# Performance work log

Hardware: AMD Instinct MI355X
Metric: run time of the kernel (lower is better)

## Reference

```python
import jax, jax.numpy as jnp
import numpy as np

B, N, D, DN, F, NUM_F, O, H = 8, 4096, 256, 128, 128, 1024, 8, 1024
EPS = 1e-5

def setup_inputs() -> dict:
    key = jax.random.key(0)
    ks = jax.random.split(key, 10)
    s = 0.02
    x = jax.random.normal(ks[0], (B, N, D), dtype=jnp.float32)
    ctx = jax.random.normal(ks[1], (B, DN), dtype=jnp.float32)
    idx = jax.random.randint(ks[2], (F,), 0, NUM_F, dtype=jnp.int64)
    cond_w = jax.random.normal(ks[3], (DN, 2 * D), dtype=jnp.float32) * s
    cond_b = jnp.zeros((2 * D,), dtype=jnp.float32)
    ffn_w_in = jax.random.normal(ks[4], (D, 2 * H), dtype=jnp.float32) * s
    ffn_b_in = jnp.zeros((2 * H,), dtype=jnp.float32)
    ffn_w_out = jax.random.normal(ks[5], (H, D), dtype=jnp.float32) * s
    ffn_b_out = jnp.zeros((D,), dtype=jnp.float32)
    emb = jax.random.normal(ks[6], (NUM_F, D * O), dtype=jnp.float32) * s
    return {"x": x, "ctx": ctx, "idx": idx, "cond_w": cond_w, "cond_b": cond_b,
            "ffn_w_in": ffn_w_in, "ffn_b_in": ffn_b_in,
            "ffn_w_out": ffn_w_out, "ffn_b_out": ffn_b_out, "emb": emb}

def reference(x, ctx, idx, cond_w, cond_b, ffn_w_in, ffn_b_in, ffn_w_out, ffn_b_out, emb):
    # Conditional LayerNorm: normalize over last dim, FiLM-style modulation from ctx
    mu = jnp.mean(x, axis=-1, keepdims=True)
    var = jnp.mean((x - mu) ** 2, axis=-1, keepdims=True)
    h = (x - mu) * jax.lax.rsqrt(var + EPS)                      # [B,N,D]
    ss = ctx @ cond_w + cond_b                                   # [B,2D]
    scale, shift = jnp.split(ss, 2, axis=-1)                     # [B,D] each
    h = h * (1.0 + scale[:, None, :]) + shift[:, None, :]
    # Gated FFN: in-proj -> (gelu(gate) * value) -> out-proj
    uv = h @ ffn_w_in + ffn_b_in                                 # [B,N,2H]
    u, v = jnp.split(uv, 2, axis=-1)
    y = (jax.nn.gelu(u) * v) @ ffn_w_out + ffn_b_out             # [B,N,D]
    # Embedding-generated per-feature output weights, then batched contraction
    w = emb[idx].reshape(F, D, O)                                # gather [F,D,O]
    out = jnp.einsum('bnd,fdo->bnfo', y, w)                      # [B,N,F,O]
    return out
```

## Files before the change

kernel.cpp:

```cpp
#include <hip/hip_runtime.h>
#include <cstdint>
#include <cstddef>

#define M_TOT 32768
#define D_    256
#define DN_   128
#define TWO_D 512
#define H_    1024
#define TWO_H 2048

typedef unsigned short ushort_t;
typedef __attribute__((ext_vector_type(8))) short bf16x8;
typedef __attribute__((ext_vector_type(4))) float f32x4;

__device__ __forceinline__ ushort_t f2bf(float f) {
  union { float f; uint32_t i; } v; v.f = f;
  uint32_t r = v.i + 0x7fffu + ((v.i >> 16) & 1u);
  return (ushort_t)(r >> 16);
}

__device__ __forceinline__ void async_ld16(const void* g, void* l) {
  __builtin_amdgcn_global_load_lds(
      (const __attribute__((address_space(1))) void*)g,
      (__attribute__((address_space(3))) void*)l, 16, 0, 0);
}

__global__ __launch_bounds__(256) void cond_ss_kernel(
    const float* __restrict__ ctx, const float* __restrict__ cond_w,
    const float* __restrict__ cond_b, float* __restrict__ ss) {
  int j = blockIdx.x * 256 + threadIdx.x;
  int b = j >> 9, col = j & 511;
  float acc = cond_b[col];
  for (int k = 0; k < DN_; ++k)
    acc += ctx[b * DN_ + k] * cond_w[k * TWO_D + col];
  ss[j] = acc;
}

__global__ __launch_bounds__(256) void prep_kernel(
    const float* __restrict__ w_in,
    const float* __restrict__ w_out,
    const float* __restrict__ emb,
    const int* __restrict__ idx,
    ushort_t* __restrict__ WinT,
    ushort_t* __restrict__ WoutT,
    ushort_t* __restrict__ W2T) {
  int id = blockIdx.x * 256 + threadIdx.x;
  if (id < 524288) {
    int n = id >> 8, k = id & 255;
    WinT[id] = f2bf(w_in[k * TWO_H + n]);
  } else if (id < 786432) {
    int t = id - 524288;
    int n = t >> 10, k = t & 1023;
    WoutT[t] = f2bf(w_out[k * D_ + n]);
  } else {
    int t = id - 786432;
    int c = t >> 8, d = t & 255;
    int f = c >> 3, o = c & 7;
    bool looks64 = (idx[1] == 0) & (idx[3] == 0) & (idx[5] == 0) & (idx[7] == 0);
    int fi = looks64 ? idx[2 * f] : idx[f];
    W2T[t] = f2bf(emb[(size_t)fi * 2048 + d * 8 + o]);
  }
}

__global__ __launch_bounds__(256) void ln_film_kernel(
    const float* __restrict__ x, const float* __restrict__ ss,
    ushort_t* __restrict__ h) {
  int row = blockIdx.x * 4 + (threadIdx.x >> 6);
  int lane = threadIdx.x & 63;
  int b = row >> 12;
  const float* xr = x + (size_t)row * D_;
  float4 pk = *(const float4*)(xr + lane * 4);
  float f0 = pk.x, f1 = pk.y, f2 = pk.z, f3 = pk.w;
  float s = f0 + f1 + f2 + f3;
  float q = f0 * f0 + f1 * f1 + f2 * f2 + f3 * f3;
#pragma unroll
  for (int off = 32; off > 0; off >>= 1) {
    s += __shfl_xor(s, off, 64);
    q += __shfl_xor(q, off, 64);
  }
  float mean = s * (1.0f / 256.0f);
  float var = q * (1.0f / 256.0f) - mean * mean;
  float rs = rsqrtf(var + 1e-5f);
  int d = lane * 4;
  const float* ssb = ss + b * TWO_D;
  float o0 = (f0 - mean) * rs * (1.0f + ssb[d + 0]) + ssb[256 + d + 0];
  float o1 = (f1 - mean) * rs * (1.0f + ssb[d + 1]) + ssb[256 + d + 1];
  float o2 = (f2 - mean) * rs * (1.0f + ssb[d + 2]) + ssb[256 + d + 2];
  float o3 = (f3 - mean) * rs * (1.0f + ssb[d + 3]) + ssb[256 + d + 3];
  uint2 st;
  st.x = (uint32_t)f2bf(o0) | ((uint32_t)f2bf(o1) << 16);
  st.y = (uint32_t)f2bf(o2) | ((uint32_t)f2bf(o3) << 16);
  *(uint2*)(h + (size_t)row * D_ + lane * 4) = st;
}

template <bool BIAS, bool OUT_F32>
__global__ __launch_bounds__(256, 2) void gemm_bt_kernel(
    const ushort_t* __restrict__ A, const ushort_t* __restrict__ BT,
    const float* __restrict__ bias, void* __restrict__ Cout,
    int M, int N, int K) {
  __shared__ ushort_t As[128 * 32];
  __shared__ ushort_t Bs[128 * 32];
  const int tid = threadIdx.x, lane = tid & 63, wave = tid >> 6;
  const int wm = wave >> 1, wn = wave & 1;
  const int m0 = blockIdx.x * 128, n0 = blockIdx.y * 128;
  const int srow = lane >> 2, sch = (lane & 3) * 8;
  f32x4 acc[4][4] = {};
  for (int k0 = 0; k0 < K; k0 += 32) {
    for (int i = wave; i < 8; i += 4) {
      async_ld16(A + (size_t)(m0 + i * 16 + srow) * K + k0 + sch, &As[i * 512]);
      async_ld16(BT + (size_t)(n0 + i * 16 + srow) * K + k0 + sch, &Bs[i * 512]);
    }
    __syncthreads();
    bf16x8 a[4], b[4];
#pragma unroll
    for (int i = 0; i < 4; ++i)
      a[i] = *(const bf16x8*)&As[(wm * 64 + i * 16 + (lane & 15)) * 32 + (lane >> 4) * 8];
#pragma unroll
    for (int j = 0; j < 4; ++j)
      b[j] = *(const bf16x8*)&Bs[(wn * 64 + j * 16 + (lane & 15)) * 32 + (lane >> 4) * 8];
#pragma unroll
    for (int i = 0; i < 4; ++i)
#pragma unroll
      for (int j = 0; j < 4; ++j)
        acc[i][j] = __builtin_amdgcn_mfma_f32_16x16x32_bf16(a[i], b[j], acc[i][j], 0, 0, 0);
    __syncthreads();
  }
#pragma unroll
  for (int j = 0; j < 4; ++j) {
    int col = n0 + wn * 64 + j * 16 + (lane & 15);
    float bv = BIAS ? bias[col] : 0.0f;
#pragma unroll
    for (int i = 0; i < 4; ++i) {
      int rowb = m0 + wm * 64 + i * 16 + ((lane >> 4) << 2);
#pragma unroll
      for (int r = 0; r < 4; ++r) {
        float val = acc[i][j][r] + bv;
        if (OUT_F32)
          ((float*)Cout)[(size_t)(rowb + r) * N + col] = val;
        else
          ((ushort_t*)Cout)[(size_t)(rowb + r) * N + col] = f2bf(val);
      }
    }
  }
}

__global__ __launch_bounds__(256, 2) void gemm_gated_kernel(
    const ushort_t* __restrict__ A,
    const ushort_t* __restrict__ WinT,
    const float* __restrict__ bin,
    ushort_t* __restrict__ G) {
  __shared__ ushort_t As[128 * 32];
  __shared__ ushort_t Bus[64 * 32];
  __shared__ ushort_t Bvs[64 * 32];
  const int tid = threadIdx.x, lane = tid & 63, wave = tid >> 6;
  const int wm = wave >> 1, wn = wave & 1;
  const int m0 = blockIdx.x * 128;
  const int j0 = blockIdx.y * 64;
  const int srow = lane >> 2, sch = (lane & 3) * 8;
  const int K = 256;
  f32x4 au[4][2] = {}, av[4][2] = {};
  for (int k0 = 0; k0 < K; k0 += 32) {
    for (int i = wave; i < 8; i += 4)
      async_ld16(A + (size_t)(m0 + i * 16 + srow) * K + k0 + sch, &As[i * 512]);
    {
      int i = wave;
      async_ld16(WinT + (size_t)(j0 + i * 16 + srow) * K + k0 + sch, &Bus[i * 512]);
      async_ld16(WinT + (size_t)(1024 + j0 + i * 16 + srow) * K + k0 + sch, &Bvs[i * 512]);
    }
    __syncthreads();
    bf16x8 a[4], bu[2], bv[2];
#pragma unroll
    for (int i = 0; i < 4; ++i)
      a[i] = *(const bf16x8*)&As[(wm * 64 + i * 16 + (lane & 15)) * 32 + (lane >> 4) * 8];
#pragma unroll
    for (int j = 0; j < 2; ++j) {
      bu[j] = *(const bf16x8*)&Bus[(wn * 32 + j * 16 + (lane & 15)) * 32 + (lane >> 4) * 8];
      bv[j] = *(const bf16x8*)&Bvs[(wn * 32 + j * 16 + (lane & 15)) * 32 + (lane >> 4) * 8];
    }
#pragma unroll
    for (int i = 0; i < 4; ++i)
#pragma unroll
      for (int j = 0; j < 2; ++j) {
        au[i][j] = __builtin_amdgcn_mfma_f32_16x16x32_bf16(a[i], bu[j], au[i][j], 0, 0, 0);
        av[i][j] = __builtin_amdgcn_mfma_f32_16x16x32_bf16(a[i], bv[j], av[i][j], 0, 0, 0);
      }
    __syncthreads();
  }
#pragma unroll
  for (int j = 0; j < 2; ++j) {
    int col = j0 + wn * 32 + j * 16 + (lane & 15);
    float bub = bin[col];
    float bvb = bin[1024 + col];
#pragma unroll
    for (int i = 0; i < 4; ++i) {
      int rowb = m0 + wm * 64 + i * 16 + ((lane >> 4) << 2);
#pragma unroll
      for (int r = 0; r < 4; ++r) {
        float u = au[i][j][r] + bub;
        float v = av[i][j][r] + bvb;
        float t = 0.7978845608028654f * (u + 0.044715f * u * u * u);
        float e = __expf(2.0f * t);
        float th = 1.0f - 2.0f / (e + 1.0f);
        float gl = 0.5f * u * (1.0f + th);
        G[(size_t)(rowb + r) * 1024 + col] = f2bf(gl * v);
      }
    }
  }
}

extern "C" void kernel_launch(void* const* d_in, const int* in_sizes, int n_in,
                              void* d_out, int out_size, void* d_ws, size_t ws_size,
                              hipStream_t stream) {
  const float* x      = (const float*)d_in[0];
  const float* ctx    = (const float*)d_in[1];
  const int*   idx    = (const int*)d_in[2];
  const float* cond_w = (const float*)d_in[3];
  const float* cond_b = (const float*)d_in[4];
  const float* w_in   = (const float*)d_in[5];
  const float* b_in   = (const float*)d_in[6];
  const float* w_out  = (const float*)d_in[7];
  const float* b_out  = (const float*)d_in[8];
  const float* emb    = (const float*)d_in[9];

  char* w = (char*)d_ws;
  float* ss = (float*)w;           w += (size_t)8 * TWO_D * 4;
  ushort_t* h = (ushort_t*)w;      w += (size_t)M_TOT * D_ * 2;
  ushort_t* y = (ushort_t*)w;      w += (size_t)M_TOT * D_ * 2;
  ushort_t* WinT = (ushort_t*)w;   w += (size_t)TWO_H * D_ * 2;
  ushort_t* WoutT = (ushort_t*)w;  w += (size_t)D_ * H_ * 2;
  ushort_t* W2T = (ushort_t*)w;    w += (size_t)H_ * D_ * 2;
  ushort_t* g = (ushort_t*)d_out;

  cond_ss_kernel<<<16, 256, 0, stream>>>(ctx, cond_w, cond_b, ss);
  prep_kernel<<<4096, 256, 0, stream>>>(w_in, w_out, emb, idx, WinT, WoutT, W2T);
  ln_film_kernel<<<M_TOT / 4, 256, 0, stream>>>(x, ss, h);
  gemm_gated_kernel<<<dim3(256, 16), 256, 0, stream>>>(h, WinT, b_in, g);
  gemm_bt_kernel<true, false><<<dim3(256, 2), 256, 0, stream>>>(g, WoutT, b_out, y, M_TOT, 256, 1024);
  gemm_bt_kernel<false, true><<<dim3(256, 8), 256, 0, stream>>>(y, W2T, nullptr, d_out, M_TOT, 1024, 256);
}
```

Baseline: 317.9 us.

## Stage GEMM epilogues through LDS for vectorized stores; tile weight transposes

The GEMM and gated-GEMM epilogues now write accumulators to a padded shared-memory tile in two passes, then issue coalesced 16-byte/8-byte row-contiguous stores instead of scattered 2/4-byte column-strided stores. The weight prep kernel is split into a shared-memory tiled transpose with bf16 conversion and a per-feature embedding gather with vector stores. This targets uncoalesced global writes, which dominate the large fp32 output store, at the cost of extra LDS use and barriers that may reduce occupancy.

```diff
diff --git a/kernel.cpp b/kernel.cpp
--- a/kernel.cpp
+++ b/kernel.cpp
@@ -36,30 +36,43 @@
   ss[j] = acc;
 }
 
-__global__ __launch_bounds__(256) void prep_kernel(
-    const float* __restrict__ w_in,
-    const float* __restrict__ w_out,
-    const float* __restrict__ emb,
-    const int* __restrict__ idx,
-    ushort_t* __restrict__ WinT,
-    ushort_t* __restrict__ WoutT,
+__global__ __launch_bounds__(256) void transpose_f32_bf16_kernel(
+    const float* __restrict__ in, ushort_t* __restrict__ out, int R, int C) {
+  __shared__ float T[64 * 65];
+  int ctiles = C >> 6;
+  int bi = blockIdx.x / ctiles, bj = blockIdx.x % ctiles;
+  int r0 = bi * 64, c0 = bj * 64;
+  int tid = threadIdx.x;
+#pragma unroll
+  for (int it = 0; it < 16; ++it) {
+    int idx = it * 256 + tid;
+    int r = idx >> 6, c = idx & 63;
+    T[r * 65 + c] = in[(size_t)(r0 + r) * C + c0 + c];
+  }
+  __syncthreads();
+#pragma unroll
+  for (int it = 0; it < 8; ++it) {
+    int idx = it * 256 + tid;
+    int a = idx >> 5;
+    int b = (idx & 31) * 2;
+    uint32_t pk = (uint32_t)f2bf(T[b * 65 + a]) |
+                  ((uint32_t)f2bf(T[(b + 1) * 65 + a]) << 16);
+    *(uint32_t*)&out[(size_t)(c0 + a) * R + r0 + b] = pk;
+  }
+}
+
+__global__ __launch_bounds__(256) void gather_emb_kernel(
+    const float* __restrict__ emb, const int* __restrict__ idx,
     ushort_t* __restrict__ W2T) {
-  int id = blockIdx.x * 256 + threadIdx.x;
-  if (id < 524288) {
-    int n = id >> 8, k = id & 255;
-    WinT[id] = f2bf(w_in[k * TWO_H + n]);
-  } else if (id < 786432) {
-    int t = id - 524288;
-    int n = t >> 10, k = t & 1023;
-    WoutT[t] = f2bf(w_out[k * D_ + n]);
-  } else {
-    int t = id - 786432;
-    int c = t >> 8, d = t & 255;
-    int f = c >> 3, o = c & 7;
-    bool looks64 = (idx[1] == 0) & (idx[3] == 0) & (idx[5] == 0) & (idx[7] == 0);
-    int fi = looks64 ? idx[2 * f] : idx[f];
-    W2T[t] = f2bf(emb[(size_t)fi * 2048 + d * 8 + o]);
-  }
+  int f = blockIdx.x;
+  bool looks64 = (idx[1] == 0) & (idx[3] == 0) & (idx[5] == 0) & (idx[7] == 0);
+  int fi = looks64 ? idx[2 * f] : idx[f];
+  const float* src = emb + (size_t)fi * 2048;
+  int o = threadIdx.x >> 5, d0 = (threadIdx.x & 31) * 8;
+  ushort_t buf[8];
+#pragma unroll
+  for (int k = 0; k < 8; ++k) buf[k] = f2bf(src[(d0 + k) * 8 + o]);
+  *(bf16x8*)&W2T[(size_t)(f * 8 + o) * 256 + d0] = *(bf16x8*)buf;
 }
 
 __global__ __launch_bounds__(256) void ln_film_kernel(
@@ -100,6 +113,7 @@
     int M, int N, int K) {
   __shared__ ushort_t As[128 * 32];
   __shared__ ushort_t Bs[128 * 32];
+  __shared__ float Cs[64 * 132];
   const int tid = threadIdx.x, lane = tid & 63, wave = tid >> 6;
   const int wm = wave >> 1, wn = wave & 1;
   const int m0 = blockIdx.x * 128, n0 = blockIdx.y * 128;
@@ -126,19 +140,35 @@
     __syncthreads();
   }
 #pragma unroll
-  for (int j = 0; j < 4; ++j) {
-    int col = n0 + wn * 64 + j * 16 + (lane & 15);
-    float bv = BIAS ? bias[col] : 0.0f;
-#pragma unroll
-    for (int i = 0; i < 4; ++i) {
-      int rowb = m0 + wm * 64 + i * 16 + ((lane >> 4) << 2);
-#pragma unroll
-      for (int r = 0; r < 4; ++r) {
-        float val = acc[i][j][r] + bv;
-        if (OUT_F32)
-          ((float*)Cout)[(size_t)(rowb + r) * N + col] = val;
-        else
-          ((ushort_t*)Cout)[(size_t)(rowb + r) * N + col] = f2bf(val);
+  for (int p = 0; p < 2; ++p) {
+    __syncthreads();
+    if (wm == p) {
+#pragma unroll
+      for (int j = 0; j < 4; ++j) {
+        int col = wn * 64 + j * 16 + (lane & 15);
+        float bv = BIAS ? bias[n0 + col] : 0.0f;
+#pragma unroll
+        for (int i = 0; i < 4; ++i) {
+          int rl = i * 16 + ((lane >> 4) << 2);
+#pragma unroll
+          for (int r = 0; r < 4; ++r)
+            Cs[(rl + r) * 132 + col] = acc[i][j][r] + bv;
+        }
+      }
+    }
+    __syncthreads();
+#pragma unroll
+    for (int it = 0; it < 8; ++it) {
+      int t = it * 256 + tid;
+      int r = t >> 5, c = (t & 31) * 4;
+      float4 v = *(const float4*)&Cs[r * 132 + c];
+      size_t off = (size_t)(m0 + p * 64 + r) * N + n0 + c;
+      if (OUT_F32) {
+        *(float4*)((float*)Cout + off) = v;
+      } else {
+        ushort4 s4;
+        s4.x = f2bf(v.x); s4.y = f2bf(v.y); s4.z = f2bf(v.z); s4.w = f2bf(v.w);
+        *(ushort4*)((ushort_t*)Cout + off) = s4;
       }
     }
   }
@@ -152,6 +182,7 @@
   __shared__ ushort_t As[128 * 32];
   __shared__ ushort_t Bus[64 * 32];
   __shared__ ushort_t Bvs[64 * 32];
+  __shared__ float Cs[64 * 68];
   const int tid = threadIdx.x, lane = tid & 63, wave = tid >> 6;
   const int wm = wave >> 1, wn = wave & 1;
   const int m0 = blockIdx.x * 128;
@@ -187,23 +218,39 @@
     __syncthreads();
   }
 #pragma unroll
-  for (int j = 0; j < 2; ++j) {
-    int col = j0 + wn * 32 + j * 16 + (lane & 15);
-    float bub = bin[col];
-    float bvb = bin[1024 + col];
-#pragma unroll
-    for (int i = 0; i < 4; ++i) {
-      int rowb = m0 + wm * 64 + i * 16 + ((lane >> 4) << 2);
-#pragma unroll
-      for (int r = 0; r < 4; ++r) {
-        float u = au[i][j][r] + bub;
-        float v = av[i][j][r] + bvb;
-        float t = 0.7978845608028654f * (u + 0.044715f * u * u * u);
-        float e = __expf(2.0f * t);
-        float th = 1.0f - 2.0f / (e + 1.0f);
-        float gl = 0.5f * u * (1.0f + th);
-        G[(size_t)(rowb + r) * 1024 + col] = f2bf(gl * v);
-      }
+  for (int p = 0; p < 2; ++p) {
+    __syncthreads();
+    if (wm == p) {
+#pragma unroll
+      for (int j = 0; j < 2; ++j) {
+        int col = wn * 32 + j * 16 + (lane & 15);
+        float bub = bin[j0 + col];
+        float bvb = bin[1024 + j0 + col];
+#pragma unroll
+        for (int i = 0; i < 4; ++i) {
+          int rl = i * 16 + ((lane >> 4) << 2);
+#pragma unroll
+          for (int r = 0; r < 4; ++r) {
+            float u = au[i][j][r] + bub;
+            float v = av[i][j][r] + bvb;
+            float t = 0.7978845608028654f * (u + 0.044715f * u * u * u);
+            float e = __expf(2.0f * t);
+            float th = 1.0f - 2.0f / (e + 1.0f);
+            float gl = 0.5f * u * (1.0f + th);
+            Cs[(rl + r) * 68 + col] = gl * v;
+          }
+        }
+      }
+    }
+    __syncthreads();
+#pragma unroll
+    for (int it = 0; it < 4; ++it) {
+      int t = it * 256 + tid;
+      int r = t >> 4, c = (t & 15) * 4;
+      float4 v = *(const float4*)&Cs[r * 68 + c];
+      ushort4 s4;
+      s4.x = f2bf(v.x); s4.y = f2bf(v.y); s4.z = f2bf(v.z); s4.w = f2bf(v.w);
+      *(ushort4*)&G[(size_t)(m0 + p * 64 + r) * 1024 + j0 + c] = s4;
     }
   }
 }
@@ -232,7 +279,9 @@
   ushort_t* g = (ushort_t*)d_out;
 
   cond_ss_kernel<<<16, 256, 0, stream>>>(ctx, cond_w, cond_b, ss);
-  prep_kernel<<<4096, 256, 0, stream>>>(w_in, w_out, emb, idx, WinT, WoutT, W2T);
+  transpose_f32_bf16_kernel<<<(D_ / 64) * (TWO_H / 64), 256, 0, stream>>>(w_in, WinT, D_, TWO_H);
+  transpose_f32_bf16_kernel<<<(H_ / 64) * (D_ / 64), 256, 0, stream>>>(w_out, WoutT, H_, D_);
+  gather_emb_kernel<<<128, 256, 0, stream>>>(emb, idx, W2T);
   ln_film_kernel<<<M_TOT / 4, 256, 0, stream>>>(x, ss, h);
   gemm_gated_kernel<<<dim3(256, 16), 256, 0, stream>>>(h, WinT, b_in, g);
   gemm_bt_kernel<true, false><<<dim3(256, 2), 256, 0, stream>>>(g, WoutT, b_out, y, M_TOT, 256, 1024);
```

Result: no change. 319.3 us (+0.4%).
